# Kernel optimization log

Hardware: AMD Instinct MI355X
Metric: run time of the kernel (lower is better)

The kernel has to match this reference:

```python
import jax, jax.numpy as jnp
import numpy as np

T = 100000
HDIM = 16
UDIM = 7
HID = 64
DT = 5.0 / 60.0  # 5 minutes in hours


def setup_inputs() -> dict:
    key = jax.random.key(0)
    ks = jax.random.split(key, 12)

    def lin(k, out_d, in_d):
        # torch nn.Linear default init: U(-1/sqrt(in), 1/sqrt(in)); scale-equivalent gaussian is fine for a numeric reference
        bound = 1.0 / np.sqrt(in_d)
        return jax.random.uniform(k, (out_d, in_d), jnp.float32, -bound, bound)

    return {
        "U": jax.random.normal(ks[0], (T, UDIM), jnp.float32),
        "W1": lin(ks[1], HID, HDIM + UDIM),
        "b1": jnp.zeros((HID,), jnp.float32),
        "W2": lin(ks[2], HID, HID),
        "b2": jnp.zeros((HID,), jnp.float32),
        "W3": lin(ks[3], HDIM, HID),
        "b3": jnp.zeros((HDIM,), jnp.float32),
        "wd": lin(ks[4], 1, HDIM).reshape(HDIM),
        "bd": jnp.zeros((), jnp.float32),
        "wt": lin(ks[5], 1, HDIM).reshape(HDIM),
        "bt": jnp.zeros((), jnp.float32),
        "wc": lin(ks[6], 1, HDIM).reshape(HDIM),
        "bc": jnp.zeros((), jnp.float32),
        "h0": jnp.zeros((HDIM,), jnp.float32),
    }


def reference(U, W1, b1, W2, b2, W3, b3, wd, bd, wt, bt, wc, bc, h0):
    dt = jnp.float32(DT)

    def step(h, u):
        # readout at current state (before the Euler step), matching the torch loop order
        d = h @ wd + bd
        tx = h @ wt + bt
        ll = h @ wc + bc
        x = jnp.concatenate([h, u])                    # (HDIM+UDIM,)
        z = jnp.tanh(W1 @ x + b1)                      # (HID,)
        z = jnp.tanh(W2 @ z + b2)                      # (HID,)
        dh = W3 @ z + b3                               # (HDIM,)
        return h + dh * dt, (d, tx, ll)

    hT, (delay, taxi, loglam) = jax.lax.scan(step, h0, U)
    return delay, taxi, loglam, hT.reshape(1, HDIM)
```

## Files before the change

kernel.cpp:

```cpp
#include <hip/hip_runtime.h>

typedef float v2f __attribute__((ext_vector_type(2)));

#define T_STEPS 100000
#define UDIM 7
#define NCHUNK 1562
#define TAIL 32
#define ZSTR 68
#define ZH (64 * ZSTR)

__device__ __forceinline__ float tanh_fast(float x) {
    float e = __expf(2.0f * x);
    return 1.0f - 2.0f * __builtin_amdgcn_rcpf(e + 1.0f);
}

__device__ __forceinline__ float readlane_f(float v, int l) {
    return __int_as_float(__builtin_amdgcn_readlane(__float_as_int(v), l));
}

template <int CTRL>
__device__ __forceinline__ float dpp_f(float v) {
    return __int_as_float(__builtin_amdgcn_update_dpp(
        0, __float_as_int(v), CTRL, 0xF, 0xF, true));
}

__global__ __launch_bounds__(128) __attribute__((amdgpu_waves_per_eu(1, 1)))
void node_scan(const float* __restrict__ U,
               const float* __restrict__ W1, const float* __restrict__ b1,
               const float* __restrict__ W2, const float* __restrict__ b2,
               const float* __restrict__ W3, const float* __restrict__ b3,
               const float* __restrict__ wd, const float* __restrict__ bd,
               const float* __restrict__ wt, const float* __restrict__ bt,
               const float* __restrict__ wc, const float* __restrict__ bc,
               const float* __restrict__ h0,
               float* __restrict__ out)
{
    const int tid  = threadIdx.x;
    const int wv   = tid >> 6;
    const int lane = tid & 63;
    const int g = lane >> 2;
    const int q = lane & 3;
    const float dt = (float)(5.0 / 60.0);

    __shared__ __align__(16) float zbuf[64];
    __shared__ __align__(16) float ubuf[3 * 512];
    __shared__ __align__(16) float zhist[2 * ZH];
    __shared__ __align__(16) float cbuf[3 * 64];
    __shared__ __align__(16) float Msh[64 * 64];
    __shared__ int flg[4];

    if (tid == 0) { flg[0] = 0; flg[1] = 3; flg[2] = 0; }

    float w1h[16]; v2f W1up[3]; float W1u6 = 0.f, b1r = 0.f, b2r = 0.f;
    v2f W2p[4][8];
    float rbD = 0.f, rbT = 0.f, rbC = 0.f, rchD = 0.f, rchT = 0.f, rchC = 0.f;

    if (wv == 0) {
#pragma unroll
        for (int j = 0; j < 16; ++j) w1h[j] = W1[lane * 23 + j];
#pragma unroll
        for (int j = 0; j < 3; ++j) {
            W1up[j].x = W1[lane * 23 + 16 + 2 * j];
            W1up[j].y = W1[lane * 23 + 17 + 2 * j];
        }
        W1u6 = W1[lane * 23 + 22];
        b1r = b1[lane];
        b2r = b2[lane];
#pragma unroll
        for (int d = 0; d < 4; ++d) {
            const int orow = (g << 2) | (q ^ d);
            const float* w2r = W2 + orow * 64 + q * 16;
#pragma unroll
            for (int j = 0; j < 8; ++j) W2p[d][j] = (v2f){ w2r[2 * j], w2r[2 * j + 1] };
        }
        for (int c = 0; c < 64; ++c) {
            float acc = 0.f;
#pragma unroll
            for (int k = 0; k < 16; ++k) acc = fmaf(w1h[k], W3[k * 64 + c], acc);
            Msh[lane * 64 + c] = acc;
        }
    } else {
        float cd = 0.f, ct = 0.f, cc = 0.f;
        for (int k = 0; k < 16; ++k) {
            const float w3v = W3[k * 64 + lane];
            cd = fmaf(wd[k], w3v, cd);
            ct = fmaf(wt[k], w3v, ct);
            cc = fmaf(wc[k], w3v, cc);
        }
        cbuf[lane] = cd; cbuf[64 + lane] = ct; cbuf[128 + lane] = cc;
        rchD = bd[0]; rchT = bt[0]; rchC = bc[0];
        for (int k = 0; k < 16; ++k) {
            rbD = fmaf(wd[k], b3[k], rbD);  rchD = fmaf(wd[k], h0[k], rchD);
            rbT = fmaf(wt[k], b3[k], rbT);  rchT = fmaf(wt[k], h0[k], rchT);
            rbC = fmaf(wc[k], b3[k], rbC);  rchC = fmaf(wc[k], h0[k], rchC);
        }
        rbD *= dt; rbT *= dt; rbC *= dt;
#pragma unroll
        for (int c = 0; c < 3; ++c) {
            const int base = c * 448, dst = c * 512;
#pragma unroll
            for (int r = 0; r < UDIM; ++r) {
                int flat = r * 64 + lane;
                int s = flat / 7, cc2 = flat % 7;
                ubuf[dst + s * 8 + cc2] = U[base + flat];
            }
            ubuf[dst + lane * 8 + 7] = 0.f;
        }
    }
    __syncthreads();

    if (wv == 0) {
        v2f Mp[4][8];
#pragma unroll
        for (int d = 0; d < 4; ++d) {
            const int orow = (g << 2) | (q ^ d);
            const float* mr = Msh + orow * 64 + q * 16;
#pragma unroll
            for (int j = 0; j < 8; ++j) Mp[d][j] = (v2f){ mr[2 * j], mr[2 * j + 1] };
        }
        float m3od = 0.f;
#pragma unroll
        for (int k = 0; k < 16; ++k) m3od = fmaf(w1h[k], b3[k], m3od);
        float A = 0.f;
        for (int k = 0; k < 16; ++k) A = fmaf(w1h[k], h0[k], A);
        float zacc = 0.f;
        float uacc;
        {
            float4 ua = *(const float4*)&ubuf[0];
            float4 ub = *(const float4*)&ubuf[4];
            v2f v0 = __builtin_elementwise_fma(W1up[0], (v2f){ua.x, ua.y}, (v2f){0.f, 0.f});
            v0 = __builtin_elementwise_fma(W1up[1], (v2f){ua.z, ua.w}, v0);
            v0 = __builtin_elementwise_fma(W1up[2], (v2f){ub.x, ub.y}, v0);
            uacc = v0.x + v0.y + fmaf(W1u6, ub.z, b1r);
        }

        auto step = [&](int li, int uoff, int zbase) {
            const float z1 = tanh_fast(A + uacc);
            zbuf[lane] = z1;
            float4 s0 = *(const float4*)&zbuf[q * 16 + 0];
            float4 s1 = *(const float4*)&zbuf[q * 16 + 4];
            float4 s2 = *(const float4*)&zbuf[q * 16 + 8];
            float4 s3 = *(const float4*)&zbuf[q * 16 + 12];

            float4 una = *(const float4*)&ubuf[uoff];
            float4 unb = *(const float4*)&ubuf[uoff + 4];

            v2f e0 = {s0.x, s0.y}, e1 = {s0.z, s0.w};
            v2f e2 = {s1.x, s1.y}, e3 = {s1.z, s1.w};
            v2f e4 = {s2.x, s2.y}, e5 = {s2.z, s2.w};
            v2f e6 = {s3.x, s3.y}, e7 = {s3.z, s3.w};
            v2f c0 = {b2r, 0.f}, c1 = {0.f, 0.f}, c2 = {0.f, 0.f}, c3 = {0.f, 0.f};
            c0 = __builtin_elementwise_fma(W2p[0][0], e0, c0);
            c1 = __builtin_elementwise_fma(W2p[1][0], e0, c1);
            c2 = __builtin_elementwise_fma(W2p[2][0], e0, c2);
            c3 = __builtin_elementwise_fma(W2p[3][0], e0, c3);
            c0 = __builtin_elementwise_fma(W2p[0][1], e1, c0);
            c1 = __builtin_elementwise_fma(W2p[1][1], e1, c1);
            c2 = __builtin_elementwise_fma(W2p[2][1], e1, c2);
            c3 = __builtin_elementwise_fma(W2p[3][1], e1, c3);
            c0 = __builtin_elementwise_fma(W2p[0][2], e2, c0);
            c1 = __builtin_elementwise_fma(W2p[1][2], e2, c1);
            c2 = __builtin_elementwise_fma(W2p[2][2], e2, c2);
            c3 = __builtin_elementwise_fma(W2p[3][2], e2, c3);
            c0 = __builtin_elementwise_fma(W2p[0][3], e3, c0);
            c1 = __builtin_elementwise_fma(W2p[1][3], e3, c1);
            c2 = __builtin_elementwise_fma(W2p[2][3], e3, c2);
            c3 = __builtin_elementwise_fma(W2p[3][3], e3, c3);
            c0 = __builtin_elementwise_fma(W2p[0][4], e4, c0);
            c1 = __builtin_elementwise_fma(W2p[1][4], e4, c1);
            c2 = __builtin_elementwise_fma(W2p[2][4], e4, c2);
            c3 = __builtin_elementwise_fma(W2p[3][4], e4, c3);
            c0 = __builtin_elementwise_fma(W2p[0][5], e5, c0);
            c1 = __builtin_elementwise_fma(W2p[1][5], e5, c1);
            c2 = __builtin_elementwise_fma(W2p[2][5], e5, c2);
            c3 = __builtin_elementwise_fma(W2p[3][5], e5, c3);
            c0 = __builtin_elementwise_fma(W2p[0][6], e6, c0);
            c1 = __builtin_elementwise_fma(W2p[1][6], e6, c1);
            c2 = __builtin_elementwise_fma(W2p[2][6], e6, c2);
            c3 = __builtin_elementwise_fma(W2p[3][6], e6, c3);
            c0 = __builtin_elementwise_fma(W2p[0][7], e7, c0);
            c1 = __builtin_elementwise_fma(W2p[1][7], e7, c1);
            c2 = __builtin_elementwise_fma(W2p[2][7], e7, c2);
            c3 = __builtin_elementwise_fma(W2p[3][7], e7, c3);
            const float P0 = c0.x + c0.y;
            const float P1 = c1.x + c1.y;
            const float P2 = c2.x + c2.y;
            const float P3 = c3.x + c3.y;
            const float Q = P0 + dpp_f<0xB1>(P1) + dpp_f<0x4E>(P2) + dpp_f<0x1B>(P3);
            const float z2 = tanh_fast(Q);
            zhist[zbase + li * ZSTR + lane] = z2;
            const float* zrow = &zhist[zbase + li * ZSTR + q * 16];
            float4 t0 = *(const float4*)&zrow[0];
            float4 t1 = *(const float4*)&zrow[4];
            float4 t2 = *(const float4*)&zrow[8];
            float4 t3 = *(const float4*)&zrow[12];
            zacc += z2;

            v2f f0 = {t0.x, t0.y}, f1 = {t0.z, t0.w};
            v2f f2 = {t1.x, t1.y}, f3 = {t1.z, t1.w};
            v2f f4 = {t2.x, t2.y}, f5 = {t2.z, t2.w};
            v2f f6 = {t3.x, t3.y}, f7 = {t3.z, t3.w};
            v2f m0 = {m3od, 0.f}, m1 = {0.f, 0.f}, m2 = {0.f, 0.f}, m3 = {0.f, 0.f};
            m0 = __builtin_elementwise_fma(Mp[0][0], f0, m0);
            m1 = __builtin_elementwise_fma(Mp[1][0], f0, m1);
            m2 = __builtin_elementwise_fma(Mp[2][0], f0, m2);
            m3 = __builtin_elementwise_fma(Mp[3][0], f0, m3);
            m0 = __builtin_elementwise_fma(Mp[0][1], f1, m0);
            m1 = __builtin_elementwise_fma(Mp[1][1], f1, m1);
            m2 = __builtin_elementwise_fma(Mp[2][1], f1, m2);
            m3 = __builtin_elementwise_fma(Mp[3][1], f1, m3);
            m0 = __builtin_elementwise_fma(Mp[0][2], f2, m0);
            m1 = __builtin_elementwise_fma(Mp[1][2], f2, m1);
            m2 = __builtin_elementwise_fma(Mp[2][2], f2, m2);
            m3 = __builtin_elementwise_fma(Mp[3][2], f2, m3);
            m0 = __builtin_elementwise_fma(Mp[0][3], f3, m0);
            m1 = __builtin_elementwise_fma(Mp[1][3], f3, m1);
            m2 = __builtin_elementwise_fma(Mp[2][3], f3, m2);
            m3 = __builtin_elementwise_fma(Mp[3][3], f3, m3);
            m0 = __builtin_elementwise_fma(Mp[0][4], f4, m0);
            m1 = __builtin_elementwise_fma(Mp[1][4], f4, m1);
            m2 = __builtin_elementwise_fma(Mp[2][4], f4, m2);
            m3 = __builtin_elementwise_fma(Mp[3][4], f4, m3);
            m0 = __builtin_elementwise_fma(Mp[0][5], f5, m0);
            m1 = __builtin_elementwise_fma(Mp[1][5], f5, m1);
            m2 = __builtin_elementwise_fma(Mp[2][5], f5, m2);
            m3 = __builtin_elementwise_fma(Mp[3][5], f5, m3);
            m0 = __builtin_elementwise_fma(Mp[0][6], f6, m0);
            m1 = __builtin_elementwise_fma(Mp[1][6], f6, m1);
            m2 = __builtin_elementwise_fma(Mp[2][6], f6, m2);
            m3 = __builtin_elementwise_fma(Mp[3][6], f6, m3);
            m0 = __builtin_elementwise_fma(Mp[0][7], f7, m0);
            m1 = __builtin_elementwise_fma(Mp[1][7], f7, m1);
            m2 = __builtin_elementwise_fma(Mp[2][7], f7, m2);
            m3 = __builtin_elementwise_fma(Mp[3][7], f7, m3);
            const float R0 = m0.x + m0.y;
            const float R1 = m1.x + m1.y;
            const float R2 = m2.x + m2.y;
            const float R3 = m3.x + m3.y;
            const float R = R0 + dpp_f<0xB1>(R1) + dpp_f<0x4E>(R2) + dpp_f<0x1B>(R3);
            A = fmaf(dt, R, A);

            v2f uv = __builtin_elementwise_fma(W1up[0], (v2f){una.x, una.y}, (v2f){0.f, 0.f});
            uv = __builtin_elementwise_fma(W1up[1], (v2f){una.z, una.w}, uv);
            uv = __builtin_elementwise_fma(W1up[2], (v2f){unb.x, unb.y}, uv);
            uacc = uv.x + uv.y + fmaf(W1u6, unb.z, b1r);
        };

        for (int cb = 0; cb <= NCHUNK; ++cb) {
            const int need_staged = (cb + 2 < NCHUNK + 1) ? cb + 2 : NCHUNK + 1;
            while (__hip_atomic_load(&flg[1], __ATOMIC_ACQUIRE,
                                     __HIP_MEMORY_SCOPE_WORKGROUP) < need_staged)
                __builtin_amdgcn_s_sleep(1);
            while (__hip_atomic_load(&flg[2], __ATOMIC_ACQUIRE,
                                     __HIP_MEMORY_SCOPE_WORKGROUP) < cb - 1)
                __builtin_amdgcn_s_sleep(1);
            const int zbase = (cb & 1) * ZH;
            const int ub = (cb % 3) * 512;
            if (cb < NCHUNK) {
                const int un = ((cb + 1) % 3) * 512;
#pragma unroll 8
                for (int li = 0; li < 64; ++li) {
                    const int uoff = (li < 63) ? ub + (li + 1) * 8 : un;
                    step(li, uoff, zbase);
                }
            } else {
                for (int li = 0; li < TAIL; ++li) step(li, ub + (li + 1) * 8, zbase);
            }
            __hip_atomic_store(&flg[0], cb + 1, __ATOMIC_RELEASE,
                               __HIP_MEMORY_SCOPE_WORKGROUP);
        }

        zbuf[lane] = zacc;
        float4 za[16];
#pragma unroll
        for (int qq = 0; qq < 16; ++qq) za[qq] = *(const float4*)&zbuf[qq * 4];
        const int row = lane & 15;
        const float* w3r = W3 + row * 64;
        float h0a = 0.f, h1a = 0.f;
#pragma unroll
        for (int qq = 0; qq < 16; ++qq) {
            h0a = fmaf(w3r[4 * qq + 0], za[qq].x, h0a);
            h1a = fmaf(w3r[4 * qq + 1], za[qq].y, h1a);
            h0a = fmaf(w3r[4 * qq + 2], za[qq].z, h0a);
            h1a = fmaf(w3r[4 * qq + 3], za[qq].w, h1a);
        }
        const float hT = h0[row] + dt * (h0a + h1a) + (float)T_STEPS * dt * b3[row];
        if (lane < 16) out[3 * T_STEPS + lane] = hT;
    } else {
        for (int cb = 0; cb <= NCHUNK; ++cb) {
            while (__hip_atomic_load(&flg[0], __ATOMIC_ACQUIRE,
                                     __HIP_MEMORY_SCOPE_WORKGROUP) < cb + 1)
                __builtin_amdgcn_s_sleep(8);
            if (cb + 3 <= NCHUNK) {
                const int dst = ((cb + 3) % 3) * 512;
                const int base = (cb + 3) * 448;
#pragma unroll
                for (int r = 0; r < UDIM; ++r) {
                    int idx = base + r * 64 + lane;
                    if (idx > T_STEPS * UDIM - 1) idx = T_STEPS * UDIM - 1;
                    const float val = U[idx];
                    int flat = r * 64 + lane;
                    int s = flat / 7, c = flat % 7;
                    ubuf[dst + s * 8 + c] = val;
                }
                __hip_atomic_store(&flg[1], cb + 4, __ATOMIC_RELEASE,
                                   __HIP_MEMORY_SCOPE_WORKGROUP);
            }
            const float* zr = &zhist[(cb & 1) * ZH + lane * ZSTR];
            v2f sd = {0.f, 0.f}, st = {0.f, 0.f}, sc = {0.f, 0.f};
#pragma unroll
            for (int qq = 0; qq < 32; ++qq) {
                v2f zv = *(const v2f*)&zr[2 * qq];
                sd = __builtin_elementwise_fma(*(const v2f*)&cbuf[2 * qq],       zv, sd);
                st = __builtin_elementwise_fma(*(const v2f*)&cbuf[64 + 2 * qq],  zv, st);
                sc = __builtin_elementwise_fma(*(const v2f*)&cbuf[128 + 2 * qq], zv, sc);
            }
            float Sd = sd.x + sd.y, St = st.x + st.y, Sc = sc.x + sc.y;
            const float oD = Sd, oT = St, oC = Sc;
#pragma unroll
            for (int dl = 1; dl < 64; dl <<= 1) {
                float ud = __shfl_up(Sd, dl, 64);
                float ut = __shfl_up(St, dl, 64);
                float uc = __shfl_up(Sc, dl, 64);
                if (lane >= dl) { Sd += ud; St += ut; Sc += uc; }
            }
            const int t = cb * 64 + lane;
            if (t < T_STEPS) {
                const float fl = (float)lane;
                out[t]               = fmaf(dt, Sd - oD, rchD) + fl * rbD;
                out[T_STEPS + t]     = fmaf(dt, St - oT, rchT) + fl * rbT;
                out[2 * T_STEPS + t] = fmaf(dt, Sc - oC, rchC) + fl * rbC;
            }
            rchD = fmaf(dt, readlane_f(Sd, 63), rchD) + 64.f * rbD;
            rchT = fmaf(dt, readlane_f(St, 63), rchT) + 64.f * rbT;
            rchC = fmaf(dt, readlane_f(Sc, 63), rchC) + 64.f * rbC;
            __hip_atomic_store(&flg[2], cb + 1, __ATOMIC_RELEASE,
                               __HIP_MEMORY_SCOPE_WORKGROUP);
        }
    }
}

extern "C" void kernel_launch(void* const* d_in, const int* in_sizes, int n_in,
                              void* d_out, int out_size, void* d_ws, size_t ws_size,
                              hipStream_t stream) {
    const float* U  = (const float*)d_in[0];
    const float* W1 = (const float*)d_in[1];
    const float* b1 = (const float*)d_in[2];
    const float* W2 = (const float*)d_in[3];
    const float* b2 = (const float*)d_in[4];
    const float* W3 = (const float*)d_in[5];
    const float* b3 = (const float*)d_in[6];
    const float* wd = (const float*)d_in[7];
    const float* bd = (const float*)d_in[8];
    const float* wt = (const float*)d_in[9];
    const float* bt = (const float*)d_in[10];
    const float* wc = (const float*)d_in[11];
    const float* bc = (const float*)d_in[12];
    const float* h0 = (const float*)d_in[13];
    (void)in_sizes; (void)n_in; (void)out_size; (void)d_ws; (void)ws_size;

    node_scan<<<dim3(1), dim3(128), 0, stream>>>(U, W1, b1, W2, b2, W3, b3,
                                                 wd, bd, wt, bt, wc, bc, h0,
                                                 (float*)d_out);
}
```

Measured before the change: 27.81 ms.

## Offload input projection and z2 column sums to helper wavefront

Moves the per-step W1·u input projection off the serial critical-path wavefront: the helper wave precomputes a whole chunk of these values into a new shared buffer two chunks ahead, and the main wave does a single LDS read per step. The running sum of z2 used for the final state is also moved to the helper wave as a column sum over the history buffer, and the final hT computation now runs there. This shortens the dependent per-step chain on wave 0. In exchange it adds shared memory, changes the flag handshake protocol, and puts more work on the helper wave, which could then become the bottleneck.

```diff
diff --git a/kernel.cpp b/kernel.cpp
--- a/kernel.cpp
+++ b/kernel.cpp
@@ -8,6 +8,8 @@
 #define TAIL 32
 #define ZSTR 68
 #define ZH (64 * ZSTR)
+#define UROWS 65
+#define UAB (UROWS * 64)
 
 __device__ __forceinline__ float tanh_fast(float x) {
     float e = __expf(2.0f * x);
@@ -46,40 +48,42 @@
     __shared__ __align__(16) float ubuf[3 * 512];
     __shared__ __align__(16) float zhist[2 * ZH];
     __shared__ __align__(16) float cbuf[3 * 64];
+    __shared__ __align__(16) float uab[2 * UAB];
     __shared__ __align__(16) float Msh[64 * 64];
     __shared__ int flg[4];
 
-    if (tid == 0) { flg[0] = 0; flg[1] = 3; flg[2] = 0; }
-
-    float w1h[16]; v2f W1up[3]; float W1u6 = 0.f, b1r = 0.f, b2r = 0.f;
+    if (tid == 0) { flg[0] = 0; flg[1] = 0; flg[2] = 0; }
+
+    float w1h[16]; float b2r = 0.f;
     v2f W2p[4][8];
+    v2f W1up[3]; float W1u6 = 0.f, b1l = 0.f;
     float rbD = 0.f, rbT = 0.f, rbC = 0.f, rchD = 0.f, rchT = 0.f, rchC = 0.f;
 
     if (wv == 0) {
 #pragma unroll
         for (int j = 0; j < 16; ++j) w1h[j] = W1[lane * 23 + j];
+        b2r = b2[lane];
+#pragma unroll
+        for (int d = 0; d < 4; ++d) {
+            const int orow = (g << 2) | (q ^ d);
+            const float* w2r = W2 + orow * 64 + q * 16;
+#pragma unroll
+            for (int j = 0; j < 8; ++j) W2p[d][j] = (v2f){ w2r[2 * j], w2r[2 * j + 1] };
+        }
+        for (int c = 0; c < 64; ++c) {
+            float acc = 0.f;
+#pragma unroll
+            for (int k = 0; k < 16; ++k) acc = fmaf(w1h[k], W3[k * 64 + c], acc);
+            Msh[lane * 64 + c] = acc;
+        }
+    } else {
 #pragma unroll
         for (int j = 0; j < 3; ++j) {
             W1up[j].x = W1[lane * 23 + 16 + 2 * j];
             W1up[j].y = W1[lane * 23 + 17 + 2 * j];
         }
         W1u6 = W1[lane * 23 + 22];
-        b1r = b1[lane];
-        b2r = b2[lane];
-#pragma unroll
-        for (int d = 0; d < 4; ++d) {
-            const int orow = (g << 2) | (q ^ d);
-            const float* w2r = W2 + orow * 64 + q * 16;
-#pragma unroll
-            for (int j = 0; j < 8; ++j) W2p[d][j] = (v2f){ w2r[2 * j], w2r[2 * j + 1] };
-        }
-        for (int c = 0; c < 64; ++c) {
-            float acc = 0.f;
-#pragma unroll
-            for (int k = 0; k < 16; ++k) acc = fmaf(w1h[k], W3[k * 64 + c], acc);
-            Msh[lane * 64 + c] = acc;
-        }
-    } else {
+        b1l = b1[lane];
         float cd = 0.f, ct = 0.f, cc = 0.f;
         for (int k = 0; k < 16; ++k) {
             const float w3v = W3[k * 64 + lane];
@@ -123,27 +127,20 @@
         for (int k = 0; k < 16; ++k) m3od = fmaf(w1h[k], b3[k], m3od);
         float A = 0.f;
         for (int k = 0; k < 16; ++k) A = fmaf(w1h[k], h0[k], A);
-        float zacc = 0.f;
-        float uacc;
-        {
-            float4 ua = *(const float4*)&ubuf[0];
-            float4 ub = *(const float4*)&ubuf[4];
-            v2f v0 = __builtin_elementwise_fma(W1up[0], (v2f){ua.x, ua.y}, (v2f){0.f, 0.f});
-            v0 = __builtin_elementwise_fma(W1up[1], (v2f){ua.z, ua.w}, v0);
-            v0 = __builtin_elementwise_fma(W1up[2], (v2f){ub.x, ub.y}, v0);
-            uacc = v0.x + v0.y + fmaf(W1u6, ub.z, b1r);
-        }
-
-        auto step = [&](int li, int uoff, int zbase) {
+
+        while (__hip_atomic_load(&flg[1], __ATOMIC_ACQUIRE,
+                                 __HIP_MEMORY_SCOPE_WORKGROUP) < 1)
+            __builtin_amdgcn_s_sleep(1);
+        float uacc = uab[lane];
+
+        auto step = [&](int li, int ub4, int zb4) {
             const float z1 = tanh_fast(A + uacc);
             zbuf[lane] = z1;
             float4 s0 = *(const float4*)&zbuf[q * 16 + 0];
             float4 s1 = *(const float4*)&zbuf[q * 16 + 4];
             float4 s2 = *(const float4*)&zbuf[q * 16 + 8];
             float4 s3 = *(const float4*)&zbuf[q * 16 + 12];
-
-            float4 una = *(const float4*)&ubuf[uoff];
-            float4 unb = *(const float4*)&ubuf[uoff + 4];
+            const float uacc_next = uab[ub4 + (li + 1) * 64 + lane];
 
             v2f e0 = {s0.x, s0.y}, e1 = {s0.z, s0.w};
             v2f e2 = {s1.x, s1.y}, e3 = {s1.z, s1.w};
@@ -188,13 +185,12 @@
             const float P3 = c3.x + c3.y;
             const float Q = P0 + dpp_f<0xB1>(P1) + dpp_f<0x4E>(P2) + dpp_f<0x1B>(P3);
             const float z2 = tanh_fast(Q);
-            zhist[zbase + li * ZSTR + lane] = z2;
-            const float* zrow = &zhist[zbase + li * ZSTR + q * 16];
+            zhist[zb4 + li * ZSTR + lane] = z2;
+            const float* zrow = &zhist[zb4 + li * ZSTR + q * 16];
             float4 t0 = *(const float4*)&zrow[0];
             float4 t1 = *(const float4*)&zrow[4];
             float4 t2 = *(const float4*)&zrow[8];
             float4 t3 = *(const float4*)&zrow[12];
-            zacc += z2;
 
             v2f f0 = {t0.x, t0.y}, f1 = {t0.z, t0.w};
             v2f f2 = {t1.x, t1.y}, f3 = {t1.z, t1.w};
@@ -239,54 +235,49 @@
             const float R3 = m3.x + m3.y;
             const float R = R0 + dpp_f<0xB1>(R1) + dpp_f<0x4E>(R2) + dpp_f<0x1B>(R3);
             A = fmaf(dt, R, A);
-
-            v2f uv = __builtin_elementwise_fma(W1up[0], (v2f){una.x, una.y}, (v2f){0.f, 0.f});
-            uv = __builtin_elementwise_fma(W1up[1], (v2f){una.z, una.w}, uv);
-            uv = __builtin_elementwise_fma(W1up[2], (v2f){unb.x, unb.y}, uv);
-            uacc = uv.x + uv.y + fmaf(W1u6, unb.z, b1r);
+            uacc = uacc_next;
         };
 
         for (int cb = 0; cb <= NCHUNK; ++cb) {
-            const int need_staged = (cb + 2 < NCHUNK + 1) ? cb + 2 : NCHUNK + 1;
             while (__hip_atomic_load(&flg[1], __ATOMIC_ACQUIRE,
-                                     __HIP_MEMORY_SCOPE_WORKGROUP) < need_staged)
+                                     __HIP_MEMORY_SCOPE_WORKGROUP) < cb + 1)
                 __builtin_amdgcn_s_sleep(1);
             while (__hip_atomic_load(&flg[2], __ATOMIC_ACQUIRE,
                                      __HIP_MEMORY_SCOPE_WORKGROUP) < cb - 1)
                 __builtin_amdgcn_s_sleep(1);
-            const int zbase = (cb & 1) * ZH;
-            const int ub = (cb % 3) * 512;
+            const int zb4 = (cb & 1) * ZH;
+            const int ub4 = (cb & 1) * UAB;
             if (cb < NCHUNK) {
-                const int un = ((cb + 1) % 3) * 512;
 #pragma unroll 8
-                for (int li = 0; li < 64; ++li) {
-                    const int uoff = (li < 63) ? ub + (li + 1) * 8 : un;
-                    step(li, uoff, zbase);
-                }
+                for (int li = 0; li < 64; ++li) step(li, ub4, zb4);
             } else {
-                for (int li = 0; li < TAIL; ++li) step(li, ub + (li + 1) * 8, zbase);
+                for (int li = 0; li < TAIL; ++li) step(li, ub4, zb4);
             }
             __hip_atomic_store(&flg[0], cb + 1, __ATOMIC_RELEASE,
                                __HIP_MEMORY_SCOPE_WORKGROUP);
         }
-
-        zbuf[lane] = zacc;
-        float4 za[16];
-#pragma unroll
-        for (int qq = 0; qq < 16; ++qq) za[qq] = *(const float4*)&zbuf[qq * 4];
-        const int row = lane & 15;
-        const float* w3r = W3 + row * 64;
-        float h0a = 0.f, h1a = 0.f;
-#pragma unroll
-        for (int qq = 0; qq < 16; ++qq) {
-            h0a = fmaf(w3r[4 * qq + 0], za[qq].x, h0a);
-            h1a = fmaf(w3r[4 * qq + 1], za[qq].y, h1a);
-            h0a = fmaf(w3r[4 * qq + 2], za[qq].z, h0a);
-            h1a = fmaf(w3r[4 * qq + 3], za[qq].w, h1a);
-        }
-        const float hT = h0[row] + dt * (h0a + h1a) + (float)T_STEPS * dt * b3[row];
-        if (lane < 16) out[3 * T_STEPS + lane] = hT;
     } else {
+        float vacc = 0.f;
+
+        auto uacc_chunk = [&](int c) {
+            const int par = (c & 1) * UAB;
+            const int src = (c % 3) * 512;
+            const int nxt = ((c + 1) % 3) * 512;
+            for (int li = 0; li < UROWS; ++li) {
+                const int uo = (li < 64) ? src + li * 8 : nxt;
+                float4 ua = *(const float4*)&ubuf[uo];
+                float4 ub = *(const float4*)&ubuf[uo + 4];
+                v2f uv = __builtin_elementwise_fma(W1up[0], (v2f){ua.x, ua.y}, (v2f){0.f, 0.f});
+                uv = __builtin_elementwise_fma(W1up[1], (v2f){ua.z, ua.w}, uv);
+                uv = __builtin_elementwise_fma(W1up[2], (v2f){ub.x, ub.y}, uv);
+                uab[par + li * 64 + lane] = uv.x + uv.y + fmaf(W1u6, ub.z, b1l);
+            }
+        };
+        uacc_chunk(0);
+        uacc_chunk(1);
+        __hip_atomic_store(&flg[1], 2, __ATOMIC_RELEASE,
+                           __HIP_MEMORY_SCOPE_WORKGROUP);
+
         for (int cb = 0; cb <= NCHUNK; ++cb) {
             while (__hip_atomic_load(&flg[0], __ATOMIC_ACQUIRE,
                                      __HIP_MEMORY_SCOPE_WORKGROUP) < cb + 1)
@@ -303,10 +294,19 @@
                     int s = flat / 7, c = flat % 7;
                     ubuf[dst + s * 8 + c] = val;
                 }
-                __hip_atomic_store(&flg[1], cb + 4, __ATOMIC_RELEASE,
+            }
+            if (cb + 2 <= NCHUNK) {
+                uacc_chunk(cb + 2);
+                __hip_atomic_store(&flg[1], cb + 3, __ATOMIC_RELEASE,
                                    __HIP_MEMORY_SCOPE_WORKGROUP);
             }
-            const float* zr = &zhist[(cb & 1) * ZH + lane * ZSTR];
+            const int zb4 = (cb & 1) * ZH;
+            const int ns = (cb == NCHUNK) ? TAIL : 64;
+            float colsum = 0.f;
+            for (int li = 0; li < ns; ++li) colsum += zhist[zb4 + li * ZSTR + lane];
+            vacc += colsum;
+
+            const float* zr = &zhist[zb4 + lane * ZSTR];
             v2f sd = {0.f, 0.f}, st = {0.f, 0.f}, sc = {0.f, 0.f};
 #pragma unroll
             for (int qq = 0; qq < 32; ++qq) {
@@ -336,6 +336,22 @@
             rchC = fmaf(dt, readlane_f(Sc, 63), rchC) + 64.f * rbC;
             __hip_atomic_store(&flg[2], cb + 1, __ATOMIC_RELEASE,
                                __HIP_MEMORY_SCOPE_WORKGROUP);
+        }
+
+        zbuf[lane] = vacc;
+        if (lane < 16) {
+            const float* w3r = W3 + lane * 64;
+            float h0a = 0.f, h1a = 0.f;
+#pragma unroll
+            for (int qq = 0; qq < 16; ++qq) {
+                float4 za = *(const float4*)&zbuf[qq * 4];
+                h0a = fmaf(w3r[4 * qq + 0], za.x, h0a);
+                h1a = fmaf(w3r[4 * qq + 1], za.y, h1a);
+                h0a = fmaf(w3r[4 * qq + 2], za.z, h0a);
+                h1a = fmaf(w3r[4 * qq + 3], za.w, h1a);
+            }
+            out[3 * T_STEPS + lane] =
+                h0[lane] + dt * (h0a + h1a) + (float)T_STEPS * dt * b3[lane];
         }
     }
 }
```

After: 26.41 ms. 1.05x faster.
